# Performance work log

Measured on AMD Instinct MI355X. Metric: run time of the kernel, lower is better.

## Reference

```python
import jax, jax.numpy as jnp
import numpy as np


def setup_inputs() -> dict:
    key = jax.random.key(0)
    k1, k2, k3, k4 = jax.random.split(key, 4)
    B, N, C = 32, 16384, 128
    return {
        "x": jax.random.normal(k1, (B, N, C), dtype=jnp.float32),
        "theta1": jax.random.normal(k2, (C,), dtype=jnp.float32),
        "theta2": jax.random.normal(k3, (C,), dtype=jnp.float32),
        "W": jax.random.normal(k4, (1,), dtype=jnp.float32),
    }


def reference(x, theta1, theta2, W):
    # Per-element gated attention score: exp(W * tanh(x.th1) * sigmoid(x.th2))
    term1 = jnp.tanh(jnp.einsum("bnc,c->bn", x, theta1))          # [B, N]
    term2 = jax.nn.sigmoid(jnp.einsum("bnc,c->bn", x, theta2))    # [B, N]
    atten = jnp.exp(W[0] * term1 * term2)                          # [B, N]
    # Global normalization over the entire (B, N) tensor, as in the original
    atten = atten / jnp.sum(atten)
    out = atten[..., None] * x                                     # [B, N, C]
    return out, atten
```

## Files before the change

### kernel.cpp

```cpp
#include <hip/hip_runtime.h>

#define ROWS   524288LL
#define OUT_ELEMS 67108864LL
#define CCOLS  128

__global__ __launch_bounds__(256) void gated_pass1(
    const float* __restrict__ x,
    const float* __restrict__ th1,
    const float* __restrict__ th2,
    const float* __restrict__ Wp,
    float* __restrict__ attenU,
    float* __restrict__ sumAcc)
{
    const int lane  = threadIdx.x & 63;
    const int wid   = (blockIdx.x * blockDim.x + threadIdx.x) >> 6;
    const int nwave = (gridDim.x * blockDim.x) >> 6;
    const int col4  = lane & 31;

    const float4 t1 = reinterpret_cast<const float4*>(th1)[col4];
    const float4 t2 = reinterpret_cast<const float4*>(th2)[col4];
    const float  W  = Wp[0];

    const float4* __restrict__ x4 = reinterpret_cast<const float4*>(x);
    const int nPairs = (int)(ROWS / 2);

    float localSum = 0.0f;

    for (int p = wid; p < nPairs; p += nwave) {
        float4 v = x4[(long long)p * 64 + lane];
        float d1 = v.x * t1.x + v.y * t1.y + v.z * t1.z + v.w * t1.w;
        float d2 = v.x * t2.x + v.y * t2.y + v.z * t2.z + v.w * t2.w;
        #pragma unroll
        for (int m = 16; m; m >>= 1) {
            d1 += __shfl_xor(d1, m);
            d2 += __shfl_xor(d2, m);
        }
        if ((lane & 31) == 0) {
            int row   = p * 2 + (lane >> 5);
            float th  = tanhf(d1);
            float sg  = 1.0f / (1.0f + expf(-d2));
            float a   = expf(W * th * sg);
            attenU[row] = a;
            localSum += a;
        }
    }

    localSum += __shfl_xor(localSum, 32);
    __shared__ float wsum[4];
    if ((threadIdx.x & 63) == 0) wsum[threadIdx.x >> 6] = localSum;
    __syncthreads();
    if (threadIdx.x == 0) {
        float s = wsum[0] + wsum[1] + wsum[2] + wsum[3];
        atomicAdd(sumAcc, s);
    }
}

__global__ __launch_bounds__(256) void gated_norm(
    float* __restrict__ atten,
    const float* __restrict__ sumAcc)
{
    const float S = sumAcc[0];
    const int n4 = (int)(ROWS / 4);
    int i = blockIdx.x * blockDim.x + threadIdx.x;
    float4* a4 = reinterpret_cast<float4*>(atten);
    for (; i < n4; i += gridDim.x * blockDim.x) {
        float4 v = a4[i];
        v.x /= S; v.y /= S; v.z /= S; v.w /= S;
        a4[i] = v;
    }
}

__global__ __launch_bounds__(256) void gated_pass2(
    const float* __restrict__ x,
    const float* __restrict__ atten,
    float* __restrict__ out)
{
    const long long n4 = OUT_ELEMS / 4;
    const float4* __restrict__ x4 = reinterpret_cast<const float4*>(x);
    float4* __restrict__ o4 = reinterpret_cast<float4*>(out);
    long long i = (long long)blockIdx.x * blockDim.x + threadIdx.x;
    const long long stride = (long long)gridDim.x * blockDim.x;
    for (; i < n4; i += stride) {
        float a  = atten[i >> 5];
        float4 v = x4[i];
        v.x *= a; v.y *= a; v.z *= a; v.w *= a;
        o4[i] = v;
    }
}

extern "C" void kernel_launch(void* const* d_in, const int* in_sizes, int n_in,
                              void* d_out, int out_size, void* d_ws, size_t ws_size,
                              hipStream_t stream) {
    const float* x   = (const float*)d_in[0];
    const float* th1 = (const float*)d_in[1];
    const float* th2 = (const float*)d_in[2];
    const float* W   = (const float*)d_in[3];

    float* out   = (float*)d_out;
    float* atten = out + OUT_ELEMS;
    float* sumAcc = (float*)d_ws;

    hipMemsetAsync(d_ws, 0, 256, stream);

    gated_pass1<<<2048, 256, 0, stream>>>(x, th1, th2, W, atten, sumAcc);
    gated_norm <<<512,  256, 0, stream>>>(atten, sumAcc);
    gated_pass2<<<2048, 256, 0, stream>>>(x, atten, out);
}
```

Before: 511.8 us.

## Restructure gated attention passes: row-tiled dot products, deterministic reduce, fused normalization

Pass1 now gives each block a fixed tile of 256 rows. Each 16-lane group handles one row using 8 columns per lane, and the dot products are stashed in shared memory so tanh/sigmoid/exp run once per lane instead of in a single lane per 32. Per-block partial sums replace the atomicAdd and memset and are combined by a one-block reduce kernel that also precomputes 1/S. The separate normalization kernel is removed: pass2 scales by the reciprocal, writes the normalized atten itself, and uses nontemporal stores for the output. The cost is an extra tiny launch, and multiplying by 1/S instead of dividing by S can change rounding slightly.

```diff
diff --git a/kernel.cpp b/kernel.cpp
--- a/kernel.cpp
+++ b/kernel.cpp
@@ -1,8 +1,10 @@
 #include <hip/hip_runtime.h>
 
-#define ROWS   524288LL
+#define ROWS      524288
 #define OUT_ELEMS 67108864LL
-#define CCOLS  128
+#define NBLK1     2048
+
+typedef float floatx4 __attribute__((ext_vector_type(4)));
 
 __global__ __launch_bounds__(256) void gated_pass1(
     const float* __restrict__ x,
@@ -10,81 +12,95 @@
     const float* __restrict__ th2,
     const float* __restrict__ Wp,
     float* __restrict__ attenU,
-    float* __restrict__ sumAcc)
+    float* __restrict__ partials)
 {
+    __shared__ float2 stash[4][64];
+    __shared__ float  wsum[4];
+
     const int lane  = threadIdx.x & 63;
-    const int wid   = (blockIdx.x * blockDim.x + threadIdx.x) >> 6;
-    const int nwave = (gridDim.x * blockDim.x) >> 6;
-    const int col4  = lane & 31;
+    const int wslot = threadIdx.x >> 6;
+    const int g     = lane >> 4;
+    const int sub   = lane & 15;
 
-    const float4 t1 = reinterpret_cast<const float4*>(th1)[col4];
-    const float4 t2 = reinterpret_cast<const float4*>(th2)[col4];
-    const float  W  = Wp[0];
+    const float4* __restrict__ t1v = reinterpret_cast<const float4*>(th1);
+    const float4* __restrict__ t2v = reinterpret_cast<const float4*>(th2);
+    const float4 t1a = t1v[sub * 2], t1b = t1v[sub * 2 + 1];
+    const float4 t2a = t2v[sub * 2], t2b = t2v[sub * 2 + 1];
+    const float  W   = Wp[0];
 
+    const int rowBase = blockIdx.x * 256 + wslot * 64;
     const float4* __restrict__ x4 = reinterpret_cast<const float4*>(x);
-    const int nPairs = (int)(ROWS / 2);
 
-    float localSum = 0.0f;
-
-    for (int p = wid; p < nPairs; p += nwave) {
-        float4 v = x4[(long long)p * 64 + lane];
-        float d1 = v.x * t1.x + v.y * t1.y + v.z * t1.z + v.w * t1.w;
-        float d2 = v.x * t2.x + v.y * t2.y + v.z * t2.z + v.w * t2.w;
+    #pragma unroll 4
+    for (int it = 0; it < 16; ++it) {
+        const int row = rowBase + it * 4 + g;
+        const float4 v0 = x4[(size_t)row * 32 + sub * 2];
+        const float4 v1 = x4[(size_t)row * 32 + sub * 2 + 1];
+        float d1 = v0.x*t1a.x + v0.y*t1a.y + v0.z*t1a.z + v0.w*t1a.w
+                 + v1.x*t1b.x + v1.y*t1b.y + v1.z*t1b.z + v1.w*t1b.w;
+        float d2 = v0.x*t2a.x + v0.y*t2a.y + v0.z*t2a.z + v0.w*t2a.w
+                 + v1.x*t2b.x + v1.y*t2b.y + v1.z*t2b.z + v1.w*t2b.w;
         #pragma unroll
-        for (int m = 16; m; m >>= 1) {
+        for (int m = 8; m; m >>= 1) {
             d1 += __shfl_xor(d1, m);
             d2 += __shfl_xor(d2, m);
         }
-        if ((lane & 31) == 0) {
-            int row   = p * 2 + (lane >> 5);
-            float th  = tanhf(d1);
-            float sg  = 1.0f / (1.0f + expf(-d2));
-            float a   = expf(W * th * sg);
-            attenU[row] = a;
-            localSum += a;
-        }
+        if (sub == 0) stash[wslot][it * 4 + g] = make_float2(d1, d2);
     }
+    __syncthreads();
 
-    localSum += __shfl_xor(localSum, 32);
+    const float2 s  = stash[wslot][lane];
+    const float  th = tanhf(s.x);
+    const float  sg = 1.0f / (1.0f + expf(-s.y));
+    const float  a  = expf(W * th * sg);
+    attenU[rowBase + lane] = a;
+
+    float ls = a;
+    #pragma unroll
+    for (int m = 32; m; m >>= 1) ls += __shfl_xor(ls, m);
+    if (lane == 0) wsum[wslot] = ls;
+    __syncthreads();
+    if (threadIdx.x == 0)
+        partials[blockIdx.x] = wsum[0] + wsum[1] + wsum[2] + wsum[3];
+}
+
+__global__ __launch_bounds__(256) void gated_reduce(
+    const float* __restrict__ partials,
+    float* __restrict__ sOut)
+{
     __shared__ float wsum[4];
-    if ((threadIdx.x & 63) == 0) wsum[threadIdx.x >> 6] = localSum;
+    float s = 0.0f;
+    for (int i = threadIdx.x; i < NBLK1; i += 256) s += partials[i];
+    #pragma unroll
+    for (int m = 32; m; m >>= 1) s += __shfl_xor(s, m);
+    if ((threadIdx.x & 63) == 0) wsum[threadIdx.x >> 6] = s;
     __syncthreads();
     if (threadIdx.x == 0) {
-        float s = wsum[0] + wsum[1] + wsum[2] + wsum[3];
-        atomicAdd(sumAcc, s);
-    }
-}
-
-__global__ __launch_bounds__(256) void gated_norm(
-    float* __restrict__ atten,
-    const float* __restrict__ sumAcc)
-{
-    const float S = sumAcc[0];
-    const int n4 = (int)(ROWS / 4);
-    int i = blockIdx.x * blockDim.x + threadIdx.x;
-    float4* a4 = reinterpret_cast<float4*>(atten);
-    for (; i < n4; i += gridDim.x * blockDim.x) {
-        float4 v = a4[i];
-        v.x /= S; v.y /= S; v.z /= S; v.w /= S;
-        a4[i] = v;
+        const float S = wsum[0] + wsum[1] + wsum[2] + wsum[3];
+        sOut[0] = S;
+        sOut[1] = 1.0f / S;
     }
 }
 
 __global__ __launch_bounds__(256) void gated_pass2(
     const float* __restrict__ x,
-    const float* __restrict__ atten,
-    float* __restrict__ out)
+    float* __restrict__ atten,
+    float* __restrict__ out,
+    const float* __restrict__ sOut)
 {
+    const float invS = sOut[1];
+    const floatx4* __restrict__ x4 = reinterpret_cast<const floatx4*>(x);
+    floatx4* __restrict__ o4 = reinterpret_cast<floatx4*>(out);
     const long long n4 = OUT_ELEMS / 4;
-    const float4* __restrict__ x4 = reinterpret_cast<const float4*>(x);
-    float4* __restrict__ o4 = reinterpret_cast<float4*>(out);
     long long i = (long long)blockIdx.x * blockDim.x + threadIdx.x;
     const long long stride = (long long)gridDim.x * blockDim.x;
     for (; i < n4; i += stride) {
-        float a  = atten[i >> 5];
-        float4 v = x4[i];
-        v.x *= a; v.y *= a; v.z *= a; v.w *= a;
-        o4[i] = v;
+        const int row = (int)(i >> 5);
+        const float an = atten[row] * invS;
+        floatx4 v = x4[i];
+        v *= an;
+        __builtin_nontemporal_store(v, &o4[i]);
+        if ((i & 31) == 0) atten[row] = an;
     }
 }
 
@@ -96,13 +112,12 @@
     const float* th2 = (const float*)d_in[2];
     const float* W   = (const float*)d_in[3];
 
-    float* out   = (float*)d_out;
-    float* atten = out + OUT_ELEMS;
-    float* sumAcc = (float*)d_ws;
+    float* out      = (float*)d_out;
+    float* atten    = out + OUT_ELEMS;
+    float* sOut     = (float*)d_ws;
+    float* partials = sOut + 16;
 
-    hipMemsetAsync(d_ws, 0, 256, stream);
-
-    gated_pass1<<<2048, 256, 0, stream>>>(x, th1, th2, W, atten, sumAcc);
-    gated_norm <<<512,  256, 0, stream>>>(atten, sumAcc);
-    gated_pass2<<<2048, 256, 0, stream>>>(x, atten, out);
+    gated_pass1 <<<NBLK1, 256, 0, stream>>>(x, th1, th2, W, atten, partials);
+    gated_reduce<<<1,     256, 0, stream>>>(partials, sOut);
+    gated_pass2 <<<2048,  256, 0, stream>>>(x, atten, out, sOut);
 }
```

Measured after the change: 495.2 us. 3.2% less time.
